# Kernel tuning notes

Measured on AMD Instinct MI355X. Metric: run time of the kernel, lower is better.

The kernel has to match this reference:

```python
import jax, jax.numpy as jnp
import numpy as np

IMAGE_SIZE = 256
CHUNK = 64            # faces per z-buffer scan step
LIGHT = (0.0, 0.0, 3.0)      # PointLights location
AMBIENT, DIFFUSE, SPECULAR, SHININESS = 0.5, 0.3, 0.2, 64.0  # pytorch3d defaults
EPS = 1e-8


def setup_inputs() -> dict:
    n_lat, n_lon, B = 72, 72, 2
    theta = np.linspace(0.15, np.pi - 0.15, n_lat)
    phi = np.linspace(0.0, 2.0 * np.pi, n_lon, endpoint=False)
    t, p = np.meshgrid(theta, phi, indexing='ij')
    sphere = np.stack([np.sin(t) * np.cos(p), np.cos(t), np.sin(t) * np.sin(p)], -1).reshape(-1, 3)
    idx = np.arange(n_lat * n_lon).reshape(n_lat, n_lon)
    idr = np.roll(idx, -1, axis=1)
    f1 = np.stack([idx[:-1], idx[1:], idr[:-1]], -1).reshape(-1, 3)
    f2 = np.stack([idr[:-1], idx[1:], idr[1:]], -1).reshape(-1, 3)
    faces = np.concatenate([f1, f2], 0).astype(np.int32)  # [10224, 3]
    key = jax.random.key(0)
    radii = 1.0 + 0.05 * jax.random.normal(jax.random.fold_in(key, 1), (B, sphere.shape[0], 1))
    vertices = (jnp.asarray(sphere, jnp.float32)[None] * radii).astype(jnp.float32)  # [B,V,3]
    tm = jnp.tile(jnp.eye(4, dtype=jnp.float32)[None], (B, 1, 1)).at[:, 2, 3].set(4.0)  # R=I, T=(0,0,4)
    focal = jnp.full((B, 1), 300.0, jnp.float32)
    pp = jnp.full((1, 2), IMAGE_SIZE / 2.0, jnp.float32)
    return {'vertices': vertices, 'transform_matrix': tm, 'focal_length': focal,
            'principal_point': pp, 'faces': jnp.asarray(faces)}


def _edge(ax, ay, bx, by, px, py):
    return (bx - ax) * (py - ay) - (by - ay) * (px - ax)


def _gather_tri(attr, f_v):
    # attr [B,V,C], f_v [B,P,3] -> [B,P,3,C]
    return jax.vmap(lambda a, f: a[f])(attr, f_v)


def _normalize(v):
    return v / (jnp.linalg.norm(v, axis=-1, keepdims=True) + EPS)


def _rasterize(verts_pix, faces_chunks, px, py):
    # verts_pix [B,V,3] (x_pix, y_pix, z_view); faces_chunks [n_chunks, CHUNK, 3]
    B, P = verts_pix.shape[0], px.shape[0]
    vp = jax.lax.stop_gradient(verts_pix)  # hard rasterization: face ids are non-differentiable

    def body(carry, inp):
        zbuf, fid = carry
        fchunk, off = inp
        tri = vp[:, fchunk]                      # [B,C,3,3]
        x, y, z = tri[..., 0], tri[..., 1], tri[..., 2]   # [B,C,3]
        pxb, pyb = px[None, None], py[None, None]
        w0 = _edge(x[..., 1, None], y[..., 1, None], x[..., 2, None], y[..., 2, None], pxb, pyb)
        w1 = _edge(x[..., 2, None], y[..., 2, None], x[..., 0, None], y[..., 0, None], pxb, pyb)
        w2 = _edge(x[..., 0, None], y[..., 0, None], x[..., 1, None], y[..., 1, None], pxb, pyb)
        denom = w0 + w1 + w2                     # signed twice-area, [B,C,P]
        safe = jnp.where(jnp.abs(denom) > EPS, denom, 1.0)
        b0, b1, b2 = w0 / safe, w1 / safe, w2 / safe
        zint = b0 * z[..., 0, None] + b1 * z[..., 1, None] + b2 * z[..., 2, None]
        inside = (b0 >= 0) & (b1 >= 0) & (b2 >= 0) & (jnp.abs(denom) > EPS) & (zint > 1e-4)
        zc = jnp.where(inside, zint, jnp.inf)    # [B,C,P]
        j = jnp.argmin(zc, axis=1)               # [B,P]
        best_z = jnp.take_along_axis(zc, j[:, None, :], axis=1)[:, 0]
        upd = best_z < zbuf
        zbuf = jnp.where(upd, best_z, zbuf)
        fid = jnp.where(upd, off + j.astype(jnp.int32), fid)
        return (zbuf, fid), None

    n_chunks = faces_chunks.shape[0]
    offs = (jnp.arange(n_chunks) * CHUNK).astype(jnp.int32)
    init = (jnp.full((B, P), jnp.inf, vp.dtype), jnp.zeros((B, P), jnp.int32))
    (zbuf, fid), _ = jax.lax.scan(body, init, (faces_chunks, offs))
    return zbuf, fid


def _render(vertices, transform_matrix, focal_length, principal_point, faces):
    B, V, _ = vertices.shape
    H = W = IMAGE_SIZE
    P = H * W
    R, T = transform_matrix[:, :3, :3], transform_matrix[:, :3, 3]
    # pytorch3d row-vector convention: X_view = X @ R + T
    vview = jnp.einsum('bvi,bij->bvj', vertices, R) + T[:, None]
    z = vview[..., 2]
    x_pix = focal_length * vview[..., 0] / z + principal_point[:, 0][:, None]
    y_pix = focal_length * vview[..., 1] / z + principal_point[:, 1][:, None]
    verts_pix = jnp.stack([x_pix, y_pix, z], -1)                 # [B,V,3]

    gy, gx = jnp.meshgrid(jnp.arange(H) + 0.5, jnp.arange(W) + 0.5, indexing='ij')
    px, py = gx.reshape(-1).astype(vertices.dtype), gy.reshape(-1).astype(vertices.dtype)

    F = faces.shape[0]
    Fpad = ((F + CHUNK - 1) // CHUNK) * CHUNK
    faces_pad = jnp.pad(faces, ((0, Fpad - F), (0, 0)))          # pad = degenerate (0,0,0)
    zbuf, fid = _rasterize(verts_pix, faces_pad.reshape(-1, CHUNK, 3), px, py)
    valid = jnp.isfinite(zbuf)                                   # [B,P]

    # differentiable re-computation of barycentrics for the winning face
    f_v = faces_pad.reshape(-1, 3)[fid]                          # [B,P,3]
    tp = _gather_tri(verts_pix, f_v)                             # [B,P,3,3]
    xk, yk = tp[..., 0], tp[..., 1]
    w0 = _edge(xk[..., 1], yk[..., 1], xk[..., 2], yk[..., 2], px[None], py[None])
    w1 = _edge(xk[..., 2], yk[..., 2], xk[..., 0], yk[..., 0], px[None], py[None])
    w2 = _edge(xk[..., 0], yk[..., 0], xk[..., 1], yk[..., 1], px[None], py[None])
    denom = w0 + w1 + w2
    safe = jnp.where(jnp.abs(denom) > EPS, denom, 1.0)
    bary = jnp.stack([w0, w1, w2], -1) / safe[..., None]         # [B,P,3]

    # area-weighted vertex normals
    tw = vertices[:, faces]                                      # [B,F,3,3]
    fn = jnp.cross(tw[:, :, 1] - tw[:, :, 0], tw[:, :, 2] - tw[:, :, 0])
    vn = jnp.zeros_like(vertices)
    for k in range(3):
        vn = vn.at[:, faces[:, k]].add(fn)
    vn = _normalize(vn)

    pix_pos = jnp.einsum('bpk,bpkc->bpc', bary, _gather_tri(vertices, f_v))
    pix_n = _normalize(jnp.einsum('bpk,bpkc->bpc', bary, _gather_tri(vn, f_v)))

    cam = -jnp.einsum('bj,bij->bi', T, R)                        # camera center in world
    light = jnp.asarray(LIGHT, vertices.dtype)
    L = _normalize(light - pix_pos)
    Vd = _normalize(cam[:, None] - pix_pos)
    ndl = jnp.sum(pix_n * L, -1)
    refl = 2.0 * ndl[..., None] * pix_n - L
    spec = SPECULAR * jnp.maximum(jnp.sum(refl * Vd, -1), 0.0) ** SHININESS * (ndl > 0)
    col = AMBIENT + DIFFUSE * jnp.maximum(ndl, 0.0) + spec       # white texels -> gray shading
    rgb = jnp.where(valid, col, 1.0)                             # white background
    images = jnp.broadcast_to(rgb[:, None], (B, 3, P)).reshape(B, 3, H, W) * 255.0
    alpha = valid.astype(vertices.dtype).reshape(B, 1, H, W)
    return images, alpha


def reference(vertices, transform_matrix, focal_length, principal_point, faces):
    return _render(vertices, transform_matrix, focal_length, principal_point, faces)
```

## Files before the change

kernel.cpp:

```cpp
#include <hip/hip_runtime.h>
#include <math.h>

#define IMG 256
#define PIX (IMG * IMG)
#define ZPOISON 0xAAAAAAAAAAAAAAAAull
#define FPOISON 0xAAAAAAAAu


__global__ __launch_bounds__(256) void k_fused(
    const float* __restrict__ verts, const int* __restrict__ faces,
    const float* __restrict__ tm, const float* __restrict__ focal,
    const float* __restrict__ pp, float* __restrict__ packed,
    float* __restrict__ vn, unsigned long long* __restrict__ zpk,
    int B, int F, int FP, int V) {
#pragma clang fp contract(off)
    int b = blockIdx.y;
    int wid = threadIdx.x >> 6;
    int lane = threadIdx.x & 63;
    int f = blockIdx.x * 4 + wid;
    if (f >= F) return;

    int i0 = faces[f * 3 + 0];
    int i1 = faces[f * 3 + 1];
    int i2 = faces[f * 3 + 2];
    const float* wv = verts + (size_t)b * V * 3;
    const float* tmb = tm + b * 16;
    float fo = focal[b];
    float ppx = pp[0], ppy = pp[1];

    float w0x = wv[i0 * 3 + 0], w0y = wv[i0 * 3 + 1], w0z = wv[i0 * 3 + 2];
    float w1x = wv[i1 * 3 + 0], w1y = wv[i1 * 3 + 1], w1z = wv[i1 * 3 + 2];
    float w2x = wv[i2 * 3 + 0], w2y = wv[i2 * 3 + 1], w2z = wv[i2 * 3 + 2];

#define XFORM(WX, WY, WZ, SX, SY, SZ)                                       \
    {                                                                       \
        float s0 = WX * tmb[0] + WY * tmb[4];  s0 = s0 + WZ * tmb[8];       \
        float v0 = s0 + tmb[3];                                             \
        float s1 = WX * tmb[1] + WY * tmb[5];  s1 = s1 + WZ * tmb[9];       \
        float v1 = s1 + tmb[7];                                             \
        float s2 = WX * tmb[2] + WY * tmb[6];  s2 = s2 + WZ * tmb[10];      \
        float v2 = s2 + tmb[11];                                            \
        SX = (fo * v0) / v2 + ppx;                                          \
        SY = (fo * v1) / v2 + ppy;                                          \
        SZ = v2;                                                            \
    }
    float x0, y0, z0, x1, y1, z1, x2, y2, z2;
    XFORM(w0x, w0y, w0z, x0, y0, z0)
    XFORM(w1x, w1y, w1z, x1, y1, z1)
    XFORM(w2x, w2y, w2z, x2, y2, z2)
#undef XFORM

    float ax = w1x - w0x, ay = w1y - w0y, az = w1z - w0z;
    float bx = w2x - w0x, by = w2y - w0y, bz = w2z - w0z;
    float fnx = ay * bz - az * by;
    float fny = az * bx - ax * bz;
    float fnz = ax * by - ay * bx;

    float* vnb = vn + (size_t)b * V * 3;
    if (lane < 9) {
        int k = lane / 3;
        int c = lane - k * 3;
        int vi = (k == 0) ? i0 : ((k == 1) ? i1 : i2);
        unsigned int* slot = (unsigned int*)&vnb[vi * 3 + c];
        atomicCAS(slot, FPOISON, 0u);
        float val = (c == 0) ? fnx : ((c == 1) ? fny : fnz);
        atomicAdd(&vnb[vi * 3 + c], val);
    }
    float4* pk = (float4*)(packed + ((size_t)b * FP + f) * 12);
    if (lane < 3) {
        float sx = (lane == 0) ? x0 : ((lane == 1) ? x1 : x2);
        float sy = (lane == 0) ? y0 : ((lane == 1) ? y1 : y2);
        float sz = (lane == 0) ? z0 : ((lane == 1) ? z1 : z2);
        pk[lane] = make_float4(sx, sy, sz, 0.0f);
    }

    float xmin = fminf(fminf(x0, x1), x2);
    float xmax = fmaxf(fmaxf(x0, x1), x2);
    float ymin = fminf(fminf(y0, y1), y2);
    float ymax = fmaxf(fmaxf(y0, y1), y2);
    int ix0 = (int)floorf(xmin - 0.5f); ix0 = ix0 < 0 ? 0 : ix0;
    int iy0 = (int)floorf(ymin - 0.5f); iy0 = iy0 < 0 ? 0 : iy0;
    int ix1 = (int)ceilf(xmax - 0.5f);  ix1 = ix1 > IMG - 1 ? IMG - 1 : ix1;
    int iy1 = (int)ceilf(ymax - 0.5f);  iy1 = iy1 > IMG - 1 ? IMG - 1 : iy1;
    int w = ix1 - ix0 + 1;
    int h = iy1 - iy0 + 1;
    if (w <= 0 || h <= 0) return;
    int n = w * h;

    unsigned long long* zb = zpk + (size_t)b * PIX;
    for (int i = lane; i < n; i += 64) {
        int iy = (int)((unsigned)i / (unsigned)w);
        int ix = i - iy * w;
        float px = (float)(ix0 + ix) + 0.5f;
        float py = (float)(iy0 + iy) + 0.5f;
        float e0 = (x2 - x1) * (py - y1) - (y2 - y1) * (px - x1);
        float e1 = (x0 - x2) * (py - y2) - (y0 - y2) * (px - x2);
        float e2 = (x1 - x0) * (py - y0) - (y1 - y0) * (px - x0);
        float denom = (e0 + e1) + e2;
        bool dok = fabsf(denom) > 1e-8f;
        float safe = dok ? denom : 1.0f;
        float b0 = e0 / safe;
        float b1 = e1 / safe;
        float b2 = e2 / safe;
        float zint = (b0 * z0 + b1 * z1) + b2 * z2;
        bool inside = (b0 >= 0.0f) && (b1 >= 0.0f) && (b2 >= 0.0f) &&
                      dok && (zint > 1e-4f);
        if (inside) {
            unsigned long long key =
                ~(((unsigned long long)__float_as_uint(zint) << 32) |
                  (unsigned int)f);
            atomicMax(&zb[(iy0 + iy) * IMG + (ix0 + ix)], key);
        }
    }
}

__global__ __launch_bounds__(256) void k_shade(
    const float* __restrict__ verts, const int* __restrict__ faces,
    const float* __restrict__ tm, const float* __restrict__ packed,
    const float* __restrict__ vn, const unsigned long long* __restrict__ zpk,
    float* __restrict__ out, int B, int V, int FP) {
#pragma clang fp contract(off)
    int p = blockIdx.x * blockDim.x + threadIdx.x;
    int b = blockIdx.y;
    if (p >= PIX) return;
    size_t imgbase = (size_t)b * 3 * PIX;
    size_t alphabase = (size_t)B * 3 * PIX + (size_t)b * PIX;
    unsigned long long key = zpk[(size_t)b * PIX + p];
    if (key == ZPOISON || key == 0ull) {
        out[imgbase + 0 * PIX + p] = 255.0f;
        out[imgbase + 1 * PIX + p] = 255.0f;
        out[imgbase + 2 * PIX + p] = 255.0f;
        out[alphabase + p] = 0.0f;
        return;
    }
    unsigned long long v = ~key;
    int f = (int)(v & 0xFFFFFFFFull);
    float px = (float)(p & (IMG - 1)) + 0.5f;
    float py = (float)(p >> 8) + 0.5f;
    const float4* pk = (const float4*)(packed + ((size_t)b * FP + f) * 12);
    float4 t0 = pk[0];
    float4 t1 = pk[1];
    float4 t2v = pk[2];
    float x0 = t0.x, y0 = t0.y;
    float x1 = t1.x, y1 = t1.y;
    float x2 = t2v.x, y2 = t2v.y;
    float w0 = (x2 - x1) * (py - y1) - (y2 - y1) * (px - x1);
    float w1 = (x0 - x2) * (py - y2) - (y0 - y2) * (px - x2);
    float w2 = (x1 - x0) * (py - y0) - (y1 - y0) * (px - x0);
    float denom = (w0 + w1) + w2;
    float safe = (fabsf(denom) > 1e-8f) ? denom : 1.0f;
    float b0 = w0 / safe;
    float b1 = w1 / safe;
    float b2 = w2 / safe;

    int i0 = faces[f * 3 + 0];
    int i1 = faces[f * 3 + 1];
    int i2 = faces[f * 3 + 2];
    const float* wv = verts + (size_t)b * V * 3;
    const float* vnb = vn + (size_t)b * V * 3;

    float a0 = vnb[i0 * 3 + 0], a1 = vnb[i0 * 3 + 1], a2 = vnb[i0 * 3 + 2];
    float c0 = vnb[i1 * 3 + 0], c1 = vnb[i1 * 3 + 1], c2 = vnb[i1 * 3 + 2];
    float d0 = vnb[i2 * 3 + 0], d1 = vnb[i2 * 3 + 1], d2 = vnb[i2 * 3 + 2];
    float na = sqrtf((a0 * a0 + a1 * a1) + a2 * a2) + 1e-8f;
    float nc = sqrtf((c0 * c0 + c1 * c1) + c2 * c2) + 1e-8f;
    float nd = sqrtf((d0 * d0 + d1 * d1) + d2 * d2) + 1e-8f;
    a0 = a0 / na; a1 = a1 / na; a2 = a2 / na;
    c0 = c0 / nc; c1 = c1 / nc; c2 = c2 / nc;
    d0 = d0 / nd; d1 = d1 / nd; d2 = d2 / nd;

    float pos[3], nr[3];
    for (int c = 0; c < 3; ++c) {
        pos[c] = (b0 * wv[i0 * 3 + c] + b1 * wv[i1 * 3 + c]) + b2 * wv[i2 * 3 + c];
    }
    nr[0] = (b0 * a0 + b1 * c0) + b2 * d0;
    nr[1] = (b0 * a1 + b1 * c1) + b2 * d1;
    nr[2] = (b0 * a2 + b1 * c2) + b2 * d2;
    float nl = sqrtf((nr[0] * nr[0] + nr[1] * nr[1]) + nr[2] * nr[2]) + 1e-8f;
    nr[0] = nr[0] / nl; nr[1] = nr[1] / nl; nr[2] = nr[2] / nl;

    const float* tmb = tm + b * 16;
    float T0 = tmb[3], T1 = tmb[7], T2 = tmb[11];
    float cam[3];
    for (int i = 0; i < 3; ++i)
        cam[i] = -((T0 * tmb[i * 4 + 0] + T1 * tmb[i * 4 + 1]) + T2 * tmb[i * 4 + 2]);

    float Lx = 0.0f - pos[0], Ly = 0.0f - pos[1], Lz = 3.0f - pos[2];
    float Ln = sqrtf((Lx * Lx + Ly * Ly) + Lz * Lz) + 1e-8f;
    Lx = Lx / Ln; Ly = Ly / Ln; Lz = Lz / Ln;
    float Vx = cam[0] - pos[0], Vy = cam[1] - pos[1], Vz = cam[2] - pos[2];
    float Vn2 = sqrtf((Vx * Vx + Vy * Vy) + Vz * Vz) + 1e-8f;
    Vx = Vx / Vn2; Vy = Vy / Vn2; Vz = Vz / Vn2;

    float ndl = (nr[0] * Lx + nr[1] * Ly) + nr[2] * Lz;
    float t2 = 2.0f * ndl;
    float rx = (t2 * nr[0]) - Lx;
    float ry = (t2 * nr[1]) - Ly;
    float rz = (t2 * nr[2]) - Lz;
    float rv = (rx * Vx + ry * Vy) + rz * Vz;
    float sp = powf(fmaxf(rv, 0.0f), 64.0f);
    float spec = (0.2f * sp) * ((ndl > 0.0f) ? 1.0f : 0.0f);
    float col = (0.5f + 0.3f * fmaxf(ndl, 0.0f)) + spec;
    col = col * 255.0f;
    out[imgbase + 0 * PIX + p] = col;
    out[imgbase + 1 * PIX + p] = col;
    out[imgbase + 2 * PIX + p] = col;
    out[alphabase + p] = 1.0f;
}

extern "C" void kernel_launch(void* const* d_in, const int* in_sizes, int n_in,
                              void* d_out, int out_size, void* d_ws, size_t ws_size,
                              hipStream_t stream) {
    const float* verts = (const float*)d_in[0];
    const float* tm    = (const float*)d_in[1];
    const float* focal = (const float*)d_in[2];
    const float* pp    = (const float*)d_in[3];
    const int*   faces = (const int*)d_in[4];

    int B = in_sizes[1] / 16;
    int V = in_sizes[0] / (3 * B);
    int F = in_sizes[4] / 3;
    int FP = ((F + 255) / 256) * 256;

    float* out = (float*)d_out;

    unsigned long long* zpk = (unsigned long long*)d_ws;
    float* vn     = (float*)(zpk + (size_t)B * PIX);
    float* packed = vn + (size_t)B * V * 3;

    k_fused<<<dim3((F + 3) / 4, B), dim3(256), 0, stream>>>(
        verts, faces, tm, focal, pp, packed, vn, zpk, B, F, FP, V);
    k_shade<<<dim3(PIX / 256, B), dim3(256), 0, stream>>>(
        verts, faces, tm, packed, vn, zpk, out, B, V, FP);
}
```

Measured before the change: 80.69 us.

## Replace per-pixel atomic z-buffer with tile binning and per-tile depth resolve

The face kernel no longer rasterizes pixels with 64-bit atomicMax. Instead it appends each face id to per-16x16-tile lists using an atomic counter. A new tile kernel stages batches of face vertices in shared memory, and each pixel thread keeps a running min depth key in registers before shading. This removes global atomics on the z-buffer, at the cost of redundant per-pixel edge tests over every face in a tile's list. It also adds a fixed per-tile list capacity of 2048 that silently truncates if exceeded.

```diff
diff --git a/kernel.cpp b/kernel.cpp
--- a/kernel.cpp
+++ b/kernel.cpp
@@ -3,16 +3,18 @@
 
 #define IMG 256
 #define PIX (IMG * IMG)
-#define ZPOISON 0xAAAAAAAAAAAAAAAAull
-#define FPOISON 0xAAAAAAAAu
-
-
-__global__ __launch_bounds__(256) void k_fused(
+#define NTILE 256
+#define CAP 2048
+#define POISON32 0xAAAAAAAAu
+#define SENT64 0xFFFFFFFFFFFFFFFFull
+
+
+__global__ __launch_bounds__(256) void k_face(
     const float* __restrict__ verts, const int* __restrict__ faces,
     const float* __restrict__ tm, const float* __restrict__ focal,
     const float* __restrict__ pp, float* __restrict__ packed,
-    float* __restrict__ vn, unsigned long long* __restrict__ zpk,
-    int B, int F, int FP, int V) {
+    float* __restrict__ vn, unsigned int* __restrict__ counts,
+    unsigned int* __restrict__ lists, int B, int F, int FP, int V) {
 #pragma clang fp contract(off)
     int b = blockIdx.y;
     int wid = threadIdx.x >> 6;
@@ -62,11 +64,11 @@
         int c = lane - k * 3;
         int vi = (k == 0) ? i0 : ((k == 1) ? i1 : i2);
         unsigned int* slot = (unsigned int*)&vnb[vi * 3 + c];
-        atomicCAS(slot, FPOISON, 0u);
+        atomicCAS(slot, POISON32, 0u);
         float val = (c == 0) ? fnx : ((c == 1) ? fny : fnz);
         atomicAdd(&vnb[vi * 3 + c], val);
     }
-    float4* pk = (float4*)(packed + ((size_t)b * FP + f) * 12);
+    float4* pk = (float4*)packed + ((size_t)b * FP + f) * 3;
     if (lane < 3) {
         float sx = (lane == 0) ? x0 : ((lane == 1) ? x1 : x2);
         float sy = (lane == 0) ? y0 : ((lane == 1) ? y1 : y2);
@@ -82,65 +84,102 @@
     int iy0 = (int)floorf(ymin - 0.5f); iy0 = iy0 < 0 ? 0 : iy0;
     int ix1 = (int)ceilf(xmax - 0.5f);  ix1 = ix1 > IMG - 1 ? IMG - 1 : ix1;
     int iy1 = (int)ceilf(ymax - 0.5f);  iy1 = iy1 > IMG - 1 ? IMG - 1 : iy1;
-    int w = ix1 - ix0 + 1;
-    int h = iy1 - iy0 + 1;
-    if (w <= 0 || h <= 0) return;
-    int n = w * h;
-
-    unsigned long long* zb = zpk + (size_t)b * PIX;
-    for (int i = lane; i < n; i += 64) {
-        int iy = (int)((unsigned)i / (unsigned)w);
-        int ix = i - iy * w;
-        float px = (float)(ix0 + ix) + 0.5f;
-        float py = (float)(iy0 + iy) + 0.5f;
-        float e0 = (x2 - x1) * (py - y1) - (y2 - y1) * (px - x1);
-        float e1 = (x0 - x2) * (py - y2) - (y0 - y2) * (px - x2);
-        float e2 = (x1 - x0) * (py - y0) - (y1 - y0) * (px - x0);
-        float denom = (e0 + e1) + e2;
-        bool dok = fabsf(denom) > 1e-8f;
-        float safe = dok ? denom : 1.0f;
-        float b0 = e0 / safe;
-        float b1 = e1 / safe;
-        float b2 = e2 / safe;
-        float zint = (b0 * z0 + b1 * z1) + b2 * z2;
-        bool inside = (b0 >= 0.0f) && (b1 >= 0.0f) && (b2 >= 0.0f) &&
-                      dok && (zint > 1e-4f);
-        if (inside) {
-            unsigned long long key =
-                ~(((unsigned long long)__float_as_uint(zint) << 32) |
-                  (unsigned int)f);
-            atomicMax(&zb[(iy0 + iy) * IMG + (ix0 + ix)], key);
-        }
+    if (ix1 < ix0 || iy1 < iy0) return;
+
+    int tx0 = ix0 >> 4, tx1 = ix1 >> 4;
+    int ty0 = iy0 >> 4, ty1 = iy1 >> 4;
+    int ntx = tx1 - tx0 + 1;
+    int nt = ntx * (ty1 - ty0 + 1);
+    for (int t = lane; t < nt; t += 64) {
+        int tyy = t / ntx;
+        int txx = t - tyy * ntx;
+        int slot = b * NTILE + (ty0 + tyy) * 16 + (tx0 + txx);
+        atomicCAS(&counts[slot], POISON32, 0u);
+        unsigned int r = atomicAdd(&counts[slot], 1u);
+        if (r < CAP) lists[(size_t)slot * CAP + r] = (unsigned int)f;
     }
 }
 
-__global__ __launch_bounds__(256) void k_shade(
+__global__ __launch_bounds__(256) void k_tile(
     const float* __restrict__ verts, const int* __restrict__ faces,
     const float* __restrict__ tm, const float* __restrict__ packed,
-    const float* __restrict__ vn, const unsigned long long* __restrict__ zpk,
-    float* __restrict__ out, int B, int V, int FP) {
+    const float* __restrict__ vn, const unsigned int* __restrict__ counts,
+    const unsigned int* __restrict__ lists, float* __restrict__ out,
+    int B, int V, int FP) {
 #pragma clang fp contract(off)
-    int p = blockIdx.x * blockDim.x + threadIdx.x;
     int b = blockIdx.y;
-    if (p >= PIX) return;
+    int tile = blockIdx.x;
+    int tid = threadIdx.x;
+    int pxi = (tile & 15) * 16 + (tid & 15);
+    int pyi = (tile >> 4) * 16 + (tid >> 4);
+    float px = (float)pxi + 0.5f;
+    float py = (float)pyi + 0.5f;
+
+    int slot = b * NTILE + tile;
+    unsigned int cnt = counts[slot];
+    if (cnt == POISON32) cnt = 0;
+    if (cnt > CAP) cnt = CAP;
+
+    const float4* pk4 = (const float4*)packed;
+    __shared__ unsigned int sid[64];
+    __shared__ float4 sf[64 * 3];
+
+    unsigned long long best = SENT64;
+    for (unsigned int base = 0; base < cnt; base += 64) {
+        int m = (int)(cnt - base);
+        if (m > 64) m = 64;
+        if (tid < m) sid[tid] = lists[(size_t)slot * CAP + base + tid];
+        __syncthreads();
+        for (int e = tid; e < m * 3; e += 256) {
+            int s = e / 3;
+            int c = e - s * 3;
+            sf[e] = pk4[((size_t)b * FP + sid[s]) * 3 + c];
+        }
+        __syncthreads();
+        for (int s = 0; s < m; ++s) {
+            float4 t0 = sf[s * 3 + 0];
+            float4 t1 = sf[s * 3 + 1];
+            float4 t2 = sf[s * 3 + 2];
+            float x0 = t0.x, y0 = t0.y, z0 = t0.z;
+            float x1 = t1.x, y1 = t1.y, z1 = t1.z;
+            float x2 = t2.x, y2 = t2.y, z2 = t2.z;
+            float e0 = (x2 - x1) * (py - y1) - (y2 - y1) * (px - x1);
+            float e1 = (x0 - x2) * (py - y2) - (y0 - y2) * (px - x2);
+            float e2 = (x1 - x0) * (py - y0) - (y1 - y0) * (px - x0);
+            float denom = (e0 + e1) + e2;
+            bool dok = fabsf(denom) > 1e-8f;
+            float safe = dok ? denom : 1.0f;
+            float b0 = e0 / safe;
+            float b1 = e1 / safe;
+            float b2 = e2 / safe;
+            float zint = (b0 * z0 + b1 * z1) + b2 * z2;
+            bool inside = (b0 >= 0.0f) && (b1 >= 0.0f) && (b2 >= 0.0f) &&
+                          dok && (zint > 1e-4f);
+            if (inside) {
+                unsigned long long key =
+                    ((unsigned long long)__float_as_uint(zint) << 32) |
+                    sid[s];
+                if (key < best) best = key;
+            }
+        }
+        __syncthreads();
+    }
+
+    int p = pyi * IMG + pxi;
     size_t imgbase = (size_t)b * 3 * PIX;
     size_t alphabase = (size_t)B * 3 * PIX + (size_t)b * PIX;
-    unsigned long long key = zpk[(size_t)b * PIX + p];
-    if (key == ZPOISON || key == 0ull) {
+    if (best == SENT64) {
         out[imgbase + 0 * PIX + p] = 255.0f;
         out[imgbase + 1 * PIX + p] = 255.0f;
         out[imgbase + 2 * PIX + p] = 255.0f;
         out[alphabase + p] = 0.0f;
         return;
     }
-    unsigned long long v = ~key;
-    int f = (int)(v & 0xFFFFFFFFull);
-    float px = (float)(p & (IMG - 1)) + 0.5f;
-    float py = (float)(p >> 8) + 0.5f;
-    const float4* pk = (const float4*)(packed + ((size_t)b * FP + f) * 12);
-    float4 t0 = pk[0];
-    float4 t1 = pk[1];
-    float4 t2v = pk[2];
+    int f = (int)(best & 0xFFFFFFFFull);
+    const float4* pkw = pk4 + ((size_t)b * FP + f) * 3;
+    float4 t0 = pkw[0];
+    float4 t1 = pkw[1];
+    float4 t2v = pkw[2];
     float x0 = t0.x, y0 = t0.y;
     float x1 = t1.x, y1 = t1.y;
     float x2 = t2v.x, y2 = t2v.y;
@@ -224,12 +263,13 @@
 
     float* out = (float*)d_out;
 
-    unsigned long long* zpk = (unsigned long long*)d_ws;
-    float* vn     = (float*)(zpk + (size_t)B * PIX);
+    float* vn = (float*)d_ws;
     float* packed = vn + (size_t)B * V * 3;
-
-    k_fused<<<dim3((F + 3) / 4, B), dim3(256), 0, stream>>>(
-        verts, faces, tm, focal, pp, packed, vn, zpk, B, F, FP, V);
-    k_shade<<<dim3(PIX / 256, B), dim3(256), 0, stream>>>(
-        verts, faces, tm, packed, vn, zpk, out, B, V, FP);
+    unsigned int* counts = (unsigned int*)(packed + (size_t)B * FP * 12);
+    unsigned int* lists = counts + (size_t)B * NTILE;
+
+    k_face<<<dim3((F + 3) / 4, B), dim3(256), 0, stream>>>(
+        verts, faces, tm, focal, pp, packed, vn, counts, lists, B, F, FP, V);
+    k_tile<<<dim3(NTILE, B), dim3(256), 0, stream>>>(
+        verts, faces, tm, packed, vn, counts, lists, out, B, V, FP);
 }
```

Result: slower. 301.0 us (+273.0%).

## Privatize vertex-normal accumulation into 8 copies and pre-check z before atomicMax

Applied to the files above, without the earlier changes.

Vertex-normal scatter now goes to one of 8 replicated accumulation buffers chosen by block index. This spreads out atomic contention, and the per-slot CAS trick for lazy poison-to-zero initialization is replaced by an explicit memset. The shading kernel sums the 8 copies when it gathers normals. The z-buffer update first does a plain read and skips the atomicMax when the key cannot win, cutting atomic traffic. The costs are an extra memset launch, 8x more normal storage, and 8x more gather loads per shaded pixel.

```diff
diff --git a/kernel.cpp b/kernel.cpp
--- a/kernel.cpp
+++ b/kernel.cpp
@@ -3,15 +3,15 @@
 
 #define IMG 256
 #define PIX (IMG * IMG)
+#define NCPY 8
 #define ZPOISON 0xAAAAAAAAAAAAAAAAull
-#define FPOISON 0xAAAAAAAAu
 
 
 __global__ __launch_bounds__(256) void k_fused(
     const float* __restrict__ verts, const int* __restrict__ faces,
     const float* __restrict__ tm, const float* __restrict__ focal,
     const float* __restrict__ pp, float* __restrict__ packed,
-    float* __restrict__ vn, unsigned long long* __restrict__ zpk,
+    float* __restrict__ vn8, unsigned long long* __restrict__ zpk,
     int B, int F, int FP, int V) {
 #pragma clang fp contract(off)
     int b = blockIdx.y;
@@ -56,17 +56,16 @@
     float fny = az * bx - ax * bz;
     float fnz = ax * by - ay * bx;
 
-    float* vnb = vn + (size_t)b * V * 3;
+    int cpy = blockIdx.x & (NCPY - 1);
+    float* vnb = vn8 + (((size_t)cpy * B + b) * V) * 3;
     if (lane < 9) {
         int k = lane / 3;
         int c = lane - k * 3;
         int vi = (k == 0) ? i0 : ((k == 1) ? i1 : i2);
-        unsigned int* slot = (unsigned int*)&vnb[vi * 3 + c];
-        atomicCAS(slot, FPOISON, 0u);
         float val = (c == 0) ? fnx : ((c == 1) ? fny : fnz);
         atomicAdd(&vnb[vi * 3 + c], val);
     }
-    float4* pk = (float4*)(packed + ((size_t)b * FP + f) * 12);
+    float4* pk = (float4*)packed + ((size_t)b * FP + f) * 3;
     if (lane < 3) {
         float sx = (lane == 0) ? x0 : ((lane == 1) ? x1 : x2);
         float sy = (lane == 0) ? y0 : ((lane == 1) ? y1 : y2);
@@ -106,10 +105,12 @@
         bool inside = (b0 >= 0.0f) && (b1 >= 0.0f) && (b2 >= 0.0f) &&
                       dok && (zint > 1e-4f);
         if (inside) {
+            int pidx = (iy0 + iy) * IMG + (ix0 + ix);
             unsigned long long key =
                 ~(((unsigned long long)__float_as_uint(zint) << 32) |
                   (unsigned int)f);
-            atomicMax(&zb[(iy0 + iy) * IMG + (ix0 + ix)], key);
+            unsigned long long cur = zb[pidx];
+            if (key > cur) atomicMax(&zb[pidx], key);
         }
     }
 }
@@ -117,7 +118,7 @@
 __global__ __launch_bounds__(256) void k_shade(
     const float* __restrict__ verts, const int* __restrict__ faces,
     const float* __restrict__ tm, const float* __restrict__ packed,
-    const float* __restrict__ vn, const unsigned long long* __restrict__ zpk,
+    const float* __restrict__ vn8, const unsigned long long* __restrict__ zpk,
     float* __restrict__ out, int B, int V, int FP) {
 #pragma clang fp contract(off)
     int p = blockIdx.x * blockDim.x + threadIdx.x;
@@ -137,7 +138,7 @@
     int f = (int)(v & 0xFFFFFFFFull);
     float px = (float)(p & (IMG - 1)) + 0.5f;
     float py = (float)(p >> 8) + 0.5f;
-    const float4* pk = (const float4*)(packed + ((size_t)b * FP + f) * 12);
+    const float4* pk = (const float4*)packed + ((size_t)b * FP + f) * 3;
     float4 t0 = pk[0];
     float4 t1 = pk[1];
     float4 t2v = pk[2];
@@ -157,11 +158,17 @@
     int i1 = faces[f * 3 + 1];
     int i2 = faces[f * 3 + 2];
     const float* wv = verts + (size_t)b * V * 3;
-    const float* vnb = vn + (size_t)b * V * 3;
-
-    float a0 = vnb[i0 * 3 + 0], a1 = vnb[i0 * 3 + 1], a2 = vnb[i0 * 3 + 2];
-    float c0 = vnb[i1 * 3 + 0], c1 = vnb[i1 * 3 + 1], c2 = vnb[i1 * 3 + 2];
-    float d0 = vnb[i2 * 3 + 0], d1 = vnb[i2 * 3 + 1], d2 = vnb[i2 * 3 + 2];
+
+    float a0 = 0.0f, a1 = 0.0f, a2 = 0.0f;
+    float c0 = 0.0f, c1 = 0.0f, c2 = 0.0f;
+    float d0 = 0.0f, d1 = 0.0f, d2 = 0.0f;
+#pragma unroll
+    for (int k = 0; k < NCPY; ++k) {
+        const float* vnb = vn8 + (((size_t)k * B + b) * V) * 3;
+        a0 += vnb[i0 * 3 + 0]; a1 += vnb[i0 * 3 + 1]; a2 += vnb[i0 * 3 + 2];
+        c0 += vnb[i1 * 3 + 0]; c1 += vnb[i1 * 3 + 1]; c2 += vnb[i1 * 3 + 2];
+        d0 += vnb[i2 * 3 + 0]; d1 += vnb[i2 * 3 + 1]; d2 += vnb[i2 * 3 + 2];
+    }
     float na = sqrtf((a0 * a0 + a1 * a1) + a2 * a2) + 1e-8f;
     float nc = sqrtf((c0 * c0 + c1 * c1) + c2 * c2) + 1e-8f;
     float nd = sqrtf((d0 * d0 + d1 * d1) + d2 * d2) + 1e-8f;
@@ -225,11 +232,12 @@
     float* out = (float*)d_out;
 
     unsigned long long* zpk = (unsigned long long*)d_ws;
-    float* vn     = (float*)(zpk + (size_t)B * PIX);
-    float* packed = vn + (size_t)B * V * 3;
-
+    float* vn8 = (float*)(zpk + (size_t)B * PIX);
+    float* packed = vn8 + (size_t)NCPY * B * V * 3;
+
+    hipMemsetAsync(vn8, 0, (size_t)NCPY * B * V * 3 * sizeof(float), stream);
     k_fused<<<dim3((F + 3) / 4, B), dim3(256), 0, stream>>>(
-        verts, faces, tm, focal, pp, packed, vn, zpk, B, F, FP, V);
+        verts, faces, tm, focal, pp, packed, vn8, zpk, B, F, FP, V);
     k_shade<<<dim3(PIX / 256, B), dim3(256), 0, stream>>>(
-        verts, faces, tm, packed, vn, zpk, out, B, V, FP);
+        verts, faces, tm, packed, vn8, zpk, out, B, V, FP);
 }
```

New measurement: 84.28 us. 4.5% more time.

## Recompute projected triangle in shade kernel, drop packed buffer, memset normals

Applied to the files above, without the earlier changes.

Removes the per-face packed screen-space vertex buffer. The shade kernel now reprojects the three world vertices itself and reuses those loaded values for position interpolation. The poison-detecting atomicCAS that zeroed each normal slot is replaced by a hipMemsetAsync of the normal buffer before the raster kernel. This trades global writes and reads plus a CAS per slot for extra per-pixel transform math and an additional memset launch.

```diff
diff --git a/kernel.cpp b/kernel.cpp
--- a/kernel.cpp
+++ b/kernel.cpp
@@ -4,15 +4,26 @@
 #define IMG 256
 #define PIX (IMG * IMG)
 #define ZPOISON 0xAAAAAAAAAAAAAAAAull
-#define FPOISON 0xAAAAAAAAu
-
+
+
+#define XFORM(TMB, FO, PPX, PPY, WX, WY, WZ, SX, SY, SZ)                    \
+    {                                                                       \
+        float s0 = WX * TMB[0] + WY * TMB[4];  s0 = s0 + WZ * TMB[8];       \
+        float v0 = s0 + TMB[3];                                             \
+        float s1 = WX * TMB[1] + WY * TMB[5];  s1 = s1 + WZ * TMB[9];       \
+        float v1 = s1 + TMB[7];                                             \
+        float s2 = WX * TMB[2] + WY * TMB[6];  s2 = s2 + WZ * TMB[10];      \
+        float v2 = s2 + TMB[11];                                            \
+        SX = (FO * v0) / v2 + PPX;                                          \
+        SY = (FO * v1) / v2 + PPY;                                          \
+        SZ = v2;                                                            \
+    }
 
 __global__ __launch_bounds__(256) void k_fused(
     const float* __restrict__ verts, const int* __restrict__ faces,
     const float* __restrict__ tm, const float* __restrict__ focal,
-    const float* __restrict__ pp, float* __restrict__ packed,
-    float* __restrict__ vn, unsigned long long* __restrict__ zpk,
-    int B, int F, int FP, int V) {
+    const float* __restrict__ pp, float* __restrict__ vn,
+    unsigned long long* __restrict__ zpk, int B, int F, int V) {
 #pragma clang fp contract(off)
     int b = blockIdx.y;
     int wid = threadIdx.x >> 6;
@@ -32,23 +43,10 @@
     float w1x = wv[i1 * 3 + 0], w1y = wv[i1 * 3 + 1], w1z = wv[i1 * 3 + 2];
     float w2x = wv[i2 * 3 + 0], w2y = wv[i2 * 3 + 1], w2z = wv[i2 * 3 + 2];
 
-#define XFORM(WX, WY, WZ, SX, SY, SZ)                                       \
-    {                                                                       \
-        float s0 = WX * tmb[0] + WY * tmb[4];  s0 = s0 + WZ * tmb[8];       \
-        float v0 = s0 + tmb[3];                                             \
-        float s1 = WX * tmb[1] + WY * tmb[5];  s1 = s1 + WZ * tmb[9];       \
-        float v1 = s1 + tmb[7];                                             \
-        float s2 = WX * tmb[2] + WY * tmb[6];  s2 = s2 + WZ * tmb[10];      \
-        float v2 = s2 + tmb[11];                                            \
-        SX = (fo * v0) / v2 + ppx;                                          \
-        SY = (fo * v1) / v2 + ppy;                                          \
-        SZ = v2;                                                            \
-    }
     float x0, y0, z0, x1, y1, z1, x2, y2, z2;
-    XFORM(w0x, w0y, w0z, x0, y0, z0)
-    XFORM(w1x, w1y, w1z, x1, y1, z1)
-    XFORM(w2x, w2y, w2z, x2, y2, z2)
-#undef XFORM
+    XFORM(tmb, fo, ppx, ppy, w0x, w0y, w0z, x0, y0, z0)
+    XFORM(tmb, fo, ppx, ppy, w1x, w1y, w1z, x1, y1, z1)
+    XFORM(tmb, fo, ppx, ppy, w2x, w2y, w2z, x2, y2, z2)
 
     float ax = w1x - w0x, ay = w1y - w0y, az = w1z - w0z;
     float bx = w2x - w0x, by = w2y - w0y, bz = w2z - w0z;
@@ -61,17 +59,8 @@
         int k = lane / 3;
         int c = lane - k * 3;
         int vi = (k == 0) ? i0 : ((k == 1) ? i1 : i2);
-        unsigned int* slot = (unsigned int*)&vnb[vi * 3 + c];
-        atomicCAS(slot, FPOISON, 0u);
         float val = (c == 0) ? fnx : ((c == 1) ? fny : fnz);
         atomicAdd(&vnb[vi * 3 + c], val);
-    }
-    float4* pk = (float4*)(packed + ((size_t)b * FP + f) * 12);
-    if (lane < 3) {
-        float sx = (lane == 0) ? x0 : ((lane == 1) ? x1 : x2);
-        float sy = (lane == 0) ? y0 : ((lane == 1) ? y1 : y2);
-        float sz = (lane == 0) ? z0 : ((lane == 1) ? z1 : z2);
-        pk[lane] = make_float4(sx, sy, sz, 0.0f);
     }
 
     float xmin = fminf(fminf(x0, x1), x2);
@@ -116,9 +105,10 @@
 
 __global__ __launch_bounds__(256) void k_shade(
     const float* __restrict__ verts, const int* __restrict__ faces,
-    const float* __restrict__ tm, const float* __restrict__ packed,
-    const float* __restrict__ vn, const unsigned long long* __restrict__ zpk,
-    float* __restrict__ out, int B, int V, int FP) {
+    const float* __restrict__ tm, const float* __restrict__ focal,
+    const float* __restrict__ pp, const float* __restrict__ vn,
+    const unsigned long long* __restrict__ zpk, float* __restrict__ out,
+    int B, int V) {
 #pragma clang fp contract(off)
     int p = blockIdx.x * blockDim.x + threadIdx.x;
     int b = blockIdx.y;
@@ -137,13 +127,26 @@
     int f = (int)(v & 0xFFFFFFFFull);
     float px = (float)(p & (IMG - 1)) + 0.5f;
     float py = (float)(p >> 8) + 0.5f;
-    const float4* pk = (const float4*)(packed + ((size_t)b * FP + f) * 12);
-    float4 t0 = pk[0];
-    float4 t1 = pk[1];
-    float4 t2v = pk[2];
-    float x0 = t0.x, y0 = t0.y;
-    float x1 = t1.x, y1 = t1.y;
-    float x2 = t2v.x, y2 = t2v.y;
+
+    int i0 = faces[f * 3 + 0];
+    int i1 = faces[f * 3 + 1];
+    int i2 = faces[f * 3 + 2];
+    const float* wv = verts + (size_t)b * V * 3;
+    const float* vnb = vn + (size_t)b * V * 3;
+    const float* tmb = tm + b * 16;
+    float fo = focal[b];
+    float ppx = pp[0], ppy = pp[1];
+
+    float w0x = wv[i0 * 3 + 0], w0y = wv[i0 * 3 + 1], w0z = wv[i0 * 3 + 2];
+    float w1x = wv[i1 * 3 + 0], w1y = wv[i1 * 3 + 1], w1z = wv[i1 * 3 + 2];
+    float w2x = wv[i2 * 3 + 0], w2y = wv[i2 * 3 + 1], w2z = wv[i2 * 3 + 2];
+
+    float x0, y0, z0u, x1, y1, z1u, x2, y2, z2u;
+    XFORM(tmb, fo, ppx, ppy, w0x, w0y, w0z, x0, y0, z0u)
+    XFORM(tmb, fo, ppx, ppy, w1x, w1y, w1z, x1, y1, z1u)
+    XFORM(tmb, fo, ppx, ppy, w2x, w2y, w2z, x2, y2, z2u)
+    (void)z0u; (void)z1u; (void)z2u;
+
     float w0 = (x2 - x1) * (py - y1) - (y2 - y1) * (px - x1);
     float w1 = (x0 - x2) * (py - y2) - (y0 - y2) * (px - x2);
     float w2 = (x1 - x0) * (py - y0) - (y1 - y0) * (px - x0);
@@ -152,12 +155,6 @@
     float b0 = w0 / safe;
     float b1 = w1 / safe;
     float b2 = w2 / safe;
-
-    int i0 = faces[f * 3 + 0];
-    int i1 = faces[f * 3 + 1];
-    int i2 = faces[f * 3 + 2];
-    const float* wv = verts + (size_t)b * V * 3;
-    const float* vnb = vn + (size_t)b * V * 3;
 
     float a0 = vnb[i0 * 3 + 0], a1 = vnb[i0 * 3 + 1], a2 = vnb[i0 * 3 + 2];
     float c0 = vnb[i1 * 3 + 0], c1 = vnb[i1 * 3 + 1], c2 = vnb[i1 * 3 + 2];
@@ -170,16 +167,15 @@
     d0 = d0 / nd; d1 = d1 / nd; d2 = d2 / nd;
 
     float pos[3], nr[3];
-    for (int c = 0; c < 3; ++c) {
-        pos[c] = (b0 * wv[i0 * 3 + c] + b1 * wv[i1 * 3 + c]) + b2 * wv[i2 * 3 + c];
-    }
+    pos[0] = (b0 * w0x + b1 * w1x) + b2 * w2x;
+    pos[1] = (b0 * w0y + b1 * w1y) + b2 * w2y;
+    pos[2] = (b0 * w0z + b1 * w1z) + b2 * w2z;
     nr[0] = (b0 * a0 + b1 * c0) + b2 * d0;
     nr[1] = (b0 * a1 + b1 * c1) + b2 * d1;
     nr[2] = (b0 * a2 + b1 * c2) + b2 * d2;
     float nl = sqrtf((nr[0] * nr[0] + nr[1] * nr[1]) + nr[2] * nr[2]) + 1e-8f;
     nr[0] = nr[0] / nl; nr[1] = nr[1] / nl; nr[2] = nr[2] / nl;
 
-    const float* tmb = tm + b * 16;
     float T0 = tmb[3], T1 = tmb[7], T2 = tmb[11];
     float cam[3];
     for (int i = 0; i < 3; ++i)
@@ -220,16 +216,15 @@
     int B = in_sizes[1] / 16;
     int V = in_sizes[0] / (3 * B);
     int F = in_sizes[4] / 3;
-    int FP = ((F + 255) / 256) * 256;
 
     float* out = (float*)d_out;
 
     unsigned long long* zpk = (unsigned long long*)d_ws;
-    float* vn     = (float*)(zpk + (size_t)B * PIX);
-    float* packed = vn + (size_t)B * V * 3;
-
+    float* vn = (float*)(zpk + (size_t)B * PIX);
+
+    hipMemsetAsync(vn, 0, (size_t)B * V * 3 * sizeof(float), stream);
     k_fused<<<dim3((F + 3) / 4, B), dim3(256), 0, stream>>>(
-        verts, faces, tm, focal, pp, packed, vn, zpk, B, F, FP, V);
+        verts, faces, tm, focal, pp, vn, zpk, B, F, V);
     k_shade<<<dim3(PIX / 256, B), dim3(256), 0, stream>>>(
-        verts, faces, tm, packed, vn, zpk, out, B, V, FP);
+        verts, faces, tm, focal, pp, vn, zpk, out, B, V);
 }
```

Result: no change. 81.21 us (+0.6%).
